# Kernel optimization log

Measured on AMD Instinct MI355X. Metric: run time of the kernel, lower is better.

## Reference

```python
import jax, jax.numpy as jnp
import numpy as np

B, D_IN, D_HID, D_OUT, E, TOP_K = 4096, 1024, 4096, 1024, 8, 2


def setup_inputs() -> dict:
    key = jax.random.key(0)
    ks = jax.random.split(key, 7)
    s_in = 1.0 / np.sqrt(D_IN)
    s_hid = 1.0 / np.sqrt(D_HID)
    return {
        "x": jax.random.normal(ks[0], (B, D_IN), jnp.float32),
        "Wg": jax.random.uniform(ks[1], (D_IN, E), jnp.float32, -s_in, s_in),
        "bg": jax.random.uniform(ks[2], (E,), jnp.float32, -s_in, s_in),
        "W1": jax.random.uniform(ks[3], (E, D_IN, D_HID), jnp.float32, -s_in, s_in),
        "b1": jax.random.uniform(ks[4], (E, D_HID), jnp.float32, -s_in, s_in),
        "W2": jax.random.uniform(ks[5], (E, D_HID, D_OUT), jnp.float32, -s_hid, s_hid),
        "b2": jax.random.uniform(ks[6], (E, D_OUT), jnp.float32, -s_hid, s_hid),
    }


def reference(x, Wg, bg, W1, b1, W2, b2):
    # Gating: [B, E]
    gate_logits = x @ Wg + bg
    # Top-k routing (values sorted descending, same as torch.topk)
    topk_logits, topk_idx = jax.lax.top_k(gate_logits, TOP_K)  # [B, K]
    topk_w = jax.nn.softmax(topk_logits, axis=-1)  # [B, K]

    # Dense per-expert FFN for all tokens (reference form of grouped GEMM)
    h = jax.nn.relu(jnp.einsum("bi,eih->beh", x, W1) + b1[None])  # [B, E, H]
    y = jnp.einsum("beh,eho->beo", h, W2) + b2[None]              # [B, E, O]

    # Gather selected experts' outputs and combine with routing weights
    y_sel = jnp.take_along_axis(y, topk_idx[:, :, None], axis=1)  # [B, K, O]
    output = jnp.sum(topk_w[:, :, None] * y_sel, axis=1)          # [B, O]

    # Load-balance auxiliary loss
    gates = jax.nn.softmax(gate_logits, axis=-1)
    expert_usage = gates.mean(axis=0)
    load_balance_loss = E * jnp.sum(expert_usage ** 2)
    return output, load_balance_loss
```

## Files before the change

kernel.cpp:

```cpp
#include <hip/hip_runtime.h>
#include <hip/hip_fp16.h>

#define BTOK  4096
#define D_IN  1024
#define D_HID 4096
#define D_OUT 1024
#define NE    8
#define PT_MAX 72
#define P_MAX  9216
#define KT1   32
#define NT1M  32
#define KT2M  128
#define NT2   8
#define GB    256

typedef _Float16 half8 __attribute__((ext_vector_type(8)));
typedef _Float16 half4v __attribute__((ext_vector_type(4)));
typedef float    floatx4 __attribute__((ext_vector_type(4)));


__device__ __forceinline__ void g2l16(const void* g, void* s) {
    __builtin_amdgcn_global_load_lds((const __attribute__((address_space(1))) void*)g,
                                     (__attribute__((address_space(3))) void*)s, 16, 0, 0);
}

__global__ __launch_bounds__(256)
void gating_kernel(const float* __restrict__ x, const float* __restrict__ Wg,
                   const float* __restrict__ bg,
                   int* __restrict__ t2i, float* __restrict__ t2w,
                   int* __restrict__ pcnt, float* __restrict__ pusage) {
    __shared__ float wgT[NE * 1024];
    __shared__ float susage[NE];
    __shared__ int   scnt[NE];
    int tid = threadIdx.x;
    if (tid < NE) { susage[tid] = 0.f; scnt[tid] = 0; }
    #pragma unroll
    for (int k = 0; k < 8192; k += 256) {
        int idx = k + tid;
        wgT[(idx & 7) * 1024 + (idx >> 3)] = Wg[idx];
    }
    __syncthreads();
    int wv = tid >> 6, lane = tid & 63;
    for (int tt = 0; tt < 4; ++tt) {
        int t = blockIdx.x * 16 + wv * 4 + tt;
        double part[NE];
        #pragma unroll
        for (int e = 0; e < NE; ++e) part[e] = 0.0;
        #pragma unroll
        for (int j = 0; j < 16; ++j) {
            int i = j * 64 + lane;
            double xv = (double)x[(size_t)t * D_IN + i];
            #pragma unroll
            for (int e = 0; e < NE; ++e) part[e] += xv * (double)wgT[e * 1024 + i];
        }
        #pragma unroll
        for (int e = 0; e < NE; ++e) {
            #pragma unroll
            for (int s = 32; s > 0; s >>= 1) part[e] += __shfl_xor(part[e], s, 64);
        }
        if (lane == 0) {
            float l[NE];
            #pragma unroll
            for (int e = 0; e < NE; ++e) l[e] = (float)part[e] + bg[e];
            float M = l[0];
            #pragma unroll
            for (int e = 1; e < NE; ++e) M = fmaxf(M, l[e]);
            float s = 0.f, g[NE];
            #pragma unroll
            for (int e = 0; e < NE; ++e) { g[e] = __expf(l[e] - M); s += g[e]; }
            float inv = 1.f / s;
            #pragma unroll
            for (int e = 0; e < NE; ++e) atomicAdd(&susage[e], g[e] * inv);
            int i0 = 0; float b0 = l[0];
            #pragma unroll
            for (int e = 1; e < NE; ++e) if (l[e] > b0) { b0 = l[e]; i0 = e; }
            int i1 = -1; float b1v = -1e30f;
            #pragma unroll
            for (int e = 0; e < NE; ++e) if (e != i0 && l[e] > b1v) { b1v = l[e]; i1 = e; }
            float w0 = 1.f / (1.f + expf(b1v - b0));
            t2i[2 * t] = i0; t2i[2 * t + 1] = i1;
            t2w[2 * t] = w0; t2w[2 * t + 1] = 1.f - w0;
            atomicAdd(&scnt[i0], 1);
            atomicAdd(&scnt[i1], 1);
        }
    }
    __syncthreads();
    if (tid < NE) {
        pcnt[blockIdx.x * NE + tid] = scnt[tid];
        pusage[blockIdx.x * NE + tid] = susage[tid];
    }
}

__global__ void scan_kernel(const int* __restrict__ pcnt, const float* __restrict__ pusage,
                            int* __restrict__ meta, float* __restrict__ out_loss) {
    int lane = threadIdx.x;
    int e = lane & 7, b0 = lane >> 3;
    int c = 0; float u = 0.f;
    for (int b = b0; b < GB; b += 8) { c += pcnt[b * 8 + e]; u += pusage[b * 8 + e]; }
    #pragma unroll
    for (int s = 8; s < 64; s <<= 1) { c += __shfl_xor(c, s, 64); u += __shfl_xor(u, s, 64); }
    int cAll[NE]; float uAll[NE];
    #pragma unroll
    for (int q = 0; q < NE; ++q) { cAll[q] = __shfl(c, q, 64); uAll[q] = __shfl(u, q, 64); }
    if (lane == 0) {
        int* cnt = meta; int* cursor = meta + 8; int* offs = meta + 16;
        int* tile2e = meta + 24; int* ntiles = meta + 96;
        int run = 0;
        for (int q = 0; q < NE; ++q) {
            cnt[q] = cAll[q];
            offs[q] = run; cursor[q] = run;
            int ntl = (cAll[q] + 127) >> 7;
            int tb = run >> 7;
            for (int i = 0; i < ntl; ++i) tile2e[tb + i] = q;
            run += ntl << 7;
        }
        ntiles[0] = run >> 7;
        float loss = 0.f;
        for (int q = 0; q < NE; ++q) { float uu = uAll[q] / (float)BTOK; loss += uu * uu; }
        out_loss[0] = (float)NE * loss;
    }
}

__global__ void fill_kernel(int* __restrict__ ptok) {
    ptok[blockIdx.x * 256 + threadIdx.x] = 0;
}

__global__ void scatter_kernel(const int* __restrict__ t2i, int* __restrict__ cursor,
                               int* __restrict__ ptok, int* __restrict__ pslot) {
    __shared__ int lcnt[NE], base[NE];
    int tid = threadIdx.x;
    if (tid < NE) lcnt[tid] = 0;
    __syncthreads();
    int t = blockIdx.x * 256 + tid;
    int e0 = t2i[2 * t], e1 = t2i[2 * t + 1];
    int l0 = atomicAdd(&lcnt[e0], 1);
    int l1 = atomicAdd(&lcnt[e1], 1);
    __syncthreads();
    if (tid < NE) base[tid] = atomicAdd(&cursor[tid], lcnt[tid]);
    __syncthreads();
    int s0 = base[e0] + l0, s1 = base[e1] + l1;
    ptok[s0] = t; ptok[s1] = t;
    pslot[2 * t] = s0; pslot[2 * t + 1] = s1;
}

__global__ void gather_x_kernel(const float* __restrict__ x, const int* __restrict__ ptok,
                                _Float16* __restrict__ xt) {
    int k0 = blockIdx.x, ptile = blockIdx.y;
    int t = threadIdx.x;
    int m = t >> 1, kb = (t & 1) * 16;
    int tok = ptok[ptile * 128 + m];
    const float* src = x + (size_t)tok * D_IN + k0 * 32 + kb;
    float4 v0 = *(const float4*)(src);
    float4 v1 = *(const float4*)(src + 4);
    float4 v2 = *(const float4*)(src + 8);
    float4 v3 = *(const float4*)(src + 12);
    half8 o0, o1;
    o0[0]=(_Float16)v0.x; o0[1]=(_Float16)v0.y; o0[2]=(_Float16)v0.z; o0[3]=(_Float16)v0.w;
    o0[4]=(_Float16)v1.x; o0[5]=(_Float16)v1.y; o0[6]=(_Float16)v1.z; o0[7]=(_Float16)v1.w;
    o1[0]=(_Float16)v2.x; o1[1]=(_Float16)v2.y; o1[2]=(_Float16)v2.z; o1[3]=(_Float16)v2.w;
    o1[4]=(_Float16)v3.x; o1[5]=(_Float16)v3.y; o1[6]=(_Float16)v3.z; o1[7]=(_Float16)v3.w;
    _Float16* dst = xt + ((size_t)ptile * KT1 + k0) * 4096 + t * 16;
    *(half8*)dst = o0;
    *(half8*)(dst + 8) = o1;
}

__global__ void wtile_kernel(const float* __restrict__ W, _Float16* __restrict__ Wt,
                             int Ktot, int Ntot, int KT, int NT) {
    int k0 = blockIdx.x, ntb = blockIdx.y, e = blockIdx.z;
    int t = threadIdx.x;
    int nl = t >> 1, kb = (t & 1) * 16;
    const float* src = W + ((size_t)e * Ktot + k0 * 32 + kb) * Ntot + ntb * 128 + nl;
    float v[16];
    #pragma unroll
    for (int j = 0; j < 16; ++j) v[j] = src[(size_t)j * Ntot];
    half8 o0, o1;
    #pragma unroll
    for (int j = 0; j < 8; ++j) { o0[j] = (_Float16)v[j]; o1[j] = (_Float16)v[j + 8]; }
    _Float16* dst = Wt + (((size_t)e * NT + ntb) * KT + k0) * 4096 + t * 16;
    *(half8*)dst = o0;
    *(half8*)(dst + 8) = o1;
}

__global__ __launch_bounds__(256, 3)
void gemm1_kernel(const _Float16* __restrict__ xt, const _Float16* __restrict__ W1t,
                  const float* __restrict__ b1, _Float16* __restrict__ ht,
                  const int* __restrict__ meta) {
    int ptile = blockIdx.x;
    if (ptile >= meta[96]) return;
    int nt = blockIdx.y;
    int e = meta[24 + ptile];

    __shared__ __align__(16) _Float16 Asm[2][128 * 32];
    __shared__ __align__(16) _Float16 Bsm[2][128 * 32];

    int tid = threadIdx.x;
    int wave = tid >> 6, lane = tid & 63;
    const _Float16* Abase = xt + (size_t)ptile * KT1 * 4096;
    const _Float16* Bbase = W1t + ((size_t)(e * NT1M + nt) * KT1) * 4096;
    int stg = wave * 512 + lane * 8;

    floatx4 acc[4][4] = {};
    int lr = lane & 15, lq = lane >> 4;
    int wm = (wave & 1) * 64, wn = (wave >> 1) * 64;

    g2l16(Abase + stg,        &Asm[0][wave * 512]);
    g2l16(Abase + stg + 2048, &Asm[0][wave * 512 + 2048]);
    g2l16(Bbase + stg,        &Bsm[0][wave * 512]);
    g2l16(Bbase + stg + 2048, &Bsm[0][wave * 512 + 2048]);
    __syncthreads();

    int ct = 0;
    for (int k0 = 0; k0 < KT1; ++k0) {
        if (k0 + 1 < KT1) {
            const _Float16* aG = Abase + (size_t)(k0 + 1) * 4096 + stg;
            const _Float16* bG = Bbase + (size_t)(k0 + 1) * 4096 + stg;
            int nb = ct ^ 1;
            g2l16(aG,        &Asm[nb][wave * 512]);
            g2l16(aG + 2048, &Asm[nb][wave * 512 + 2048]);
            g2l16(bG,        &Bsm[nb][wave * 512]);
            g2l16(bG + 2048, &Bsm[nb][wave * 512 + 2048]);
        }
        const _Float16* As = Asm[ct];
        const _Float16* Bs = Bsm[ct];
        half8 af[4], bf[4];
        #pragma unroll
        for (int f = 0; f < 4; ++f) {
            af[f] = *(const half8*)&As[(wm + f * 16 + lr) * 32 + lq * 8];
            bf[f] = *(const half8*)&Bs[(wn + f * 16 + lr) * 32 + lq * 8];
        }
        #pragma unroll
        for (int mf = 0; mf < 4; ++mf)
            #pragma unroll
            for (int nf = 0; nf < 4; ++nf)
                acc[mf][nf] = __builtin_amdgcn_mfma_f32_16x16x32_f16(af[mf], bf[nf], acc[mf][nf], 0, 0, 0);
        __syncthreads();
        ct ^= 1;
    }

    const float* b1e = b1 + (size_t)e * D_HID;
    #pragma unroll
    for (int mf = 0; mf < 4; ++mf) {
        #pragma unroll
        for (int v = 0; v < 4; ++v) {
            int m = wm + mf * 16 + lq * 4 + v;
            #pragma unroll
            for (int nf = 0; nf < 4; ++nf) {
                int hl = nt * 128 + wn + nf * 16 + lr;
                float val = acc[mf][nf][v] + b1e[hl];
                ht[((size_t)ptile * KT2M + (hl >> 5)) * 4096 + m * 32 + (hl & 31)]
                    = (_Float16)fmaxf(val, 0.f);
            }
        }
    }
}

__global__ __launch_bounds__(256, 3)
void gemm2_kernel(const _Float16* __restrict__ ht, const _Float16* __restrict__ W2t,
                  _Float16* __restrict__ y, const int* __restrict__ meta) {
    int ptile = blockIdx.x;
    if (ptile >= meta[96]) return;
    int nt = blockIdx.y;
    int e = meta[24 + ptile];

    __shared__ __align__(16) _Float16 Asm[2][128 * 32];
    __shared__ __align__(16) _Float16 Bsm[2][128 * 32];

    int tid = threadIdx.x;
    int wave = tid >> 6, lane = tid & 63;
    const _Float16* Abase = ht + (size_t)ptile * KT2M * 4096;
    const _Float16* Bbase = W2t + ((size_t)(e * NT2 + nt) * KT2M) * 4096;
    int stg = wave * 512 + lane * 8;

    floatx4 acc[4][4] = {};
    int lr = lane & 15, lq = lane >> 4;
    int wm = (wave & 1) * 64, wn = (wave >> 1) * 64;

    g2l16(Abase + stg,        &Asm[0][wave * 512]);
    g2l16(Abase + stg + 2048, &Asm[0][wave * 512 + 2048]);
    g2l16(Bbase + stg,        &Bsm[0][wave * 512]);
    g2l16(Bbase + stg + 2048, &Bsm[0][wave * 512 + 2048]);
    __syncthreads();

    int ct = 0;
    for (int k0 = 0; k0 < KT2M; ++k0) {
        if (k0 + 1 < KT2M) {
            const _Float16* aG = Abase + (size_t)(k0 + 1) * 4096 + stg;
            const _Float16* bG = Bbase + (size_t)(k0 + 1) * 4096 + stg;
            int nb = ct ^ 1;
            g2l16(aG,        &Asm[nb][wave * 512]);
            g2l16(aG + 2048, &Asm[nb][wave * 512 + 2048]);
            g2l16(bG,        &Bsm[nb][wave * 512]);
            g2l16(bG + 2048, &Bsm[nb][wave * 512 + 2048]);
        }
        const _Float16* As = Asm[ct];
        const _Float16* Bs = Bsm[ct];
        half8 af[4], bf[4];
        #pragma unroll
        for (int f = 0; f < 4; ++f) {
            af[f] = *(const half8*)&As[(wm + f * 16 + lr) * 32 + lq * 8];
            bf[f] = *(const half8*)&Bs[(wn + f * 16 + lr) * 32 + lq * 8];
        }
        #pragma unroll
        for (int mf = 0; mf < 4; ++mf)
            #pragma unroll
            for (int nf = 0; nf < 4; ++nf)
                acc[mf][nf] = __builtin_amdgcn_mfma_f32_16x16x32_f16(af[mf], bf[nf], acc[mf][nf], 0, 0, 0);
        __syncthreads();
        ct ^= 1;
    }

    #pragma unroll
    for (int mf = 0; mf < 4; ++mf) {
        #pragma unroll
        for (int v = 0; v < 4; ++v) {
            int m = wm + mf * 16 + lq * 4 + v;
            #pragma unroll
            for (int nf = 0; nf < 4; ++nf) {
                int c = nt * 128 + wn + nf * 16 + lr;
                y[(size_t)(ptile * 128 + m) * D_OUT + c] = (_Float16)acc[mf][nf][v];
            }
        }
    }
}

__global__ void combine_kernel(const _Float16* __restrict__ y, const float* __restrict__ b2,
                               const int* __restrict__ t2i, const float* __restrict__ t2w,
                               const int* __restrict__ pslot, float* __restrict__ out) {
    int t = blockIdx.x;
    int c = threadIdx.x * 4;
    int e0 = t2i[2 * t], e1 = t2i[2 * t + 1];
    float w0 = t2w[2 * t], w1 = t2w[2 * t + 1];
    size_t s0 = (size_t)pslot[2 * t] * D_OUT + c;
    size_t s1 = (size_t)pslot[2 * t + 1] * D_OUT + c;
    half4v a0 = *(const half4v*)(y + s0);
    half4v a1 = *(const half4v*)(y + s1);
    float4 bias0 = *(const float4*)(b2 + (size_t)e0 * D_OUT + c);
    float4 bias1 = *(const float4*)(b2 + (size_t)e1 * D_OUT + c);
    float4 o;
    o.x = w0 * ((float)a0[0] + bias0.x) + w1 * ((float)a1[0] + bias1.x);
    o.y = w0 * ((float)a0[1] + bias0.y) + w1 * ((float)a1[1] + bias1.y);
    o.z = w0 * ((float)a0[2] + bias0.z) + w1 * ((float)a1[2] + bias1.z);
    o.w = w0 * ((float)a0[3] + bias0.w) + w1 * ((float)a1[3] + bias1.w);
    *(float4*)(out + (size_t)t * D_OUT + c) = o;
}

extern "C" void kernel_launch(void* const* d_in, const int* in_sizes, int n_in,
                              void* d_out, int out_size, void* d_ws, size_t ws_size,
                              hipStream_t stream) {
    const float* x  = (const float*)d_in[0];
    const float* Wg = (const float*)d_in[1];
    const float* bg = (const float*)d_in[2];
    const float* W1 = (const float*)d_in[3];
    const float* b1 = (const float*)d_in[4];
    const float* W2 = (const float*)d_in[5];
    const float* b2 = (const float*)d_in[6];
    float* out = (float*)d_out;

    char* ws = (char*)d_ws;
    _Float16* xt     = (_Float16*)(ws);
    _Float16* W1t    = (_Float16*)(ws + 18874368ull);
    _Float16* W2t    = (_Float16*)(ws + 85983232ull);
    _Float16* ht     = (_Float16*)(ws + 153092096ull);
    _Float16* y      = (_Float16*)(ws + 228589568ull);
    int*      t2i    = (int*)(ws + 247463936ull);
    float*    t2w    = (float*)(ws + 247496704ull);
    int*      ptok   = (int*)(ws + 247529472ull);
    int*      pslot  = (int*)(ws + 247566336ull);
    int*      meta   = (int*)(ws + 247599104ull);
    int*      pcnt   = (int*)(ws + 247599616ull);
    float*    pusage = (float*)(ws + 247607808ull);
    int* cursor = meta + 8;

    hipMemsetAsync(meta, 0, 512, stream);

    gating_kernel<<<GB, 256, 0, stream>>>(x, Wg, bg, t2i, t2w, pcnt, pusage);
    scan_kernel<<<1, 64, 0, stream>>>(pcnt, pusage, meta, out + (size_t)BTOK * D_OUT);
    fill_kernel<<<36, 256, 0, stream>>>(ptok);
    scatter_kernel<<<16, 256, 0, stream>>>(t2i, cursor, ptok, pslot);
    gather_x_kernel<<<dim3(KT1, PT_MAX), 256, 0, stream>>>(x, ptok, xt);

    wtile_kernel<<<dim3(KT1, NT1M, 8), 256, 0, stream>>>(W1, W1t, D_IN, D_HID, KT1, NT1M);
    wtile_kernel<<<dim3(KT2M, NT2, 8), 256, 0, stream>>>(W2, W2t, D_HID, D_OUT, KT2M, NT2);

    gemm1_kernel<<<dim3(PT_MAX, NT1M), 256, 0, stream>>>(xt, W1t, b1, ht, meta);
    gemm2_kernel<<<dim3(PT_MAX, NT2), 256, 0, stream>>>(ht, W2t, y, meta);

    combine_kernel<<<BTOK, 256, 0, stream>>>(y, b2, t2i, t2w, pslot, out);
}
```

Measured before the change: 602.6 us.

## Enlarge grouped GEMM tiles to 256x256 with 8 waves and deeper pipelining

Both expert GEMMs move from 128x128 tiles with 4 waves to 256x256 tiles with 8 waves per block. Each k-step now stages 64 K-columns in two halves and prefetches two stages ahead, using explicit waitcnt/barrier control, register double-buffering of fragments and s_setprio around the MFMA bursts. Expert segments are padded to multiples of 256 rows so every macro tile belongs to one expert, and the workspace layout grows to match. The aim is more data reuse per global and LDS load and better overlap of loads with MFMAs, at the cost of more padding work, fewer blocks in the grid and higher register pressure.

Result: slower. 633.1 us (+5.1%).

```diff
diff --git a/kernel.cpp b/kernel.cpp
--- a/kernel.cpp
+++ b/kernel.cpp
@@ -6,11 +6,12 @@
 #define D_HID 4096
 #define D_OUT 1024
 #define NE    8
-#define PT_MAX 72
-#define P_MAX  9216
+#define PT_MAX 80
+#define PT2_MAX 40
+#define P_MAX  10240
 #define KT1   32
 #define NT1M  32
-#define KT2M  128
+#define KT2C  128
 #define NT2   8
 #define GB    256
 
@@ -104,12 +105,12 @@
     for (int q = 0; q < NE; ++q) { cAll[q] = __shfl(c, q, 64); uAll[q] = __shfl(u, q, 64); }
     if (lane == 0) {
         int* cnt = meta; int* cursor = meta + 8; int* offs = meta + 16;
-        int* tile2e = meta + 24; int* ntiles = meta + 96;
+        int* tile2e = meta + 24; int* ntiles = meta + 104;
         int run = 0;
         for (int q = 0; q < NE; ++q) {
             cnt[q] = cAll[q];
             offs[q] = run; cursor[q] = run;
-            int ntl = (cAll[q] + 127) >> 7;
+            int ntl = ((cAll[q] + 255) >> 8) << 1;
             int tb = run >> 7;
             for (int i = 0; i < ntl; ++i) tile2e[tb + i] = q;
             run += ntl << 7;
@@ -181,143 +182,172 @@
     *(half8*)(dst + 8) = o1;
 }
 
-__global__ __launch_bounds__(256, 3)
+template<int NKT>
+__device__ __forceinline__ void gemm_core(
+    const _Float16* __restrict__ Ab, const _Float16* __restrict__ Bb, size_t aS,
+    _Float16 (&LA)[2][2][2 * 4096], _Float16 (&LB)[2][2][2 * 4096],
+    int wave, int lane, floatx4 (&acc)[8][4])
+{
+    int wr = wave >> 2, wc = wave & 3;
+    int lr = lane & 15, lq = lane >> 4;
+    int go  = wave * 512 + lane * 8;
+    int aro = wr * 4096;
+    int bro = (wc >> 1) * 4096 + (wc & 1) * 2048;
+    int fo  = lr * 32 + lq * 8;
+
+#define STG(kt, s, h) do { \
+    const _Float16* ga_ = Ab + (size_t)((kt) * 2 + (h)) * 4096 + go; \
+    const _Float16* gb_ = Bb + (size_t)((kt) * 2 + (h)) * 4096 + go; \
+    g2l16(ga_,      &LA[s][h][wave * 512]); \
+    g2l16(ga_ + aS, &LA[s][h][4096 + wave * 512]); \
+    g2l16(gb_,      &LB[s][h][wave * 512]); \
+    g2l16(gb_ + aS, &LB[s][h][4096 + wave * 512]); \
+} while (0)
+
+    half8 af[8], bf[4];
+
+    STG(0, 0, 0); STG(0, 0, 1); STG(1, 1, 0); STG(1, 1, 1);
+    asm volatile("s_waitcnt vmcnt(8)" ::: "memory");
+    __builtin_amdgcn_s_barrier();
+    {
+        const _Float16* Ar = &LA[0][0][aro];
+        const _Float16* Br = &LB[0][0][bro];
+        #pragma unroll
+        for (int mf = 0; mf < 8; ++mf) af[mf] = *(const half8*)(Ar + mf * 512 + fo);
+        #pragma unroll
+        for (int nf = 0; nf < 4; ++nf) bf[nf] = *(const half8*)(Br + nf * 512 + fo);
+    }
+    asm volatile("s_waitcnt lgkmcnt(0)" ::: "memory");
+    __builtin_amdgcn_s_barrier();
+
+    for (int kt = 0; kt < NKT; ++kt) {
+        int s = kt & 1;
+        bool st = (kt + 2 < NKT);
+
+        if (st) STG(kt + 2, s, 0);
+        {
+            const _Float16* Ar = &LA[s][1][aro];
+            const _Float16* Br = &LB[s][1][bro];
+            __builtin_amdgcn_s_setprio(1);
+            #pragma unroll
+            for (int mf = 0; mf < 8; ++mf) {
+                #pragma unroll
+                for (int nf = 0; nf < 4; ++nf)
+                    acc[mf][nf] = __builtin_amdgcn_mfma_f32_16x16x32_f16(af[mf], bf[nf], acc[mf][nf], 0, 0, 0);
+                if (mf == 7) {
+                    #pragma unroll
+                    for (int nf = 0; nf < 4; ++nf) bf[nf] = *(const half8*)(Br + nf * 512 + fo);
+                }
+                af[mf] = *(const half8*)(Ar + mf * 512 + fo);
+            }
+            __builtin_amdgcn_s_setprio(0);
+        }
+        asm volatile("s_waitcnt lgkmcnt(0)" ::: "memory");
+        __builtin_amdgcn_s_barrier();
+
+        if (st) STG(kt + 2, s, 1);
+        bool nx = (kt + 1 < NKT);
+        if (nx) {
+            if (st) { asm volatile("s_waitcnt vmcnt(8)" ::: "memory"); }
+            else    { asm volatile("s_waitcnt vmcnt(0)" ::: "memory"); }
+        }
+        {
+            const _Float16* Ar = &LA[s ^ 1][0][aro];
+            const _Float16* Br = &LB[s ^ 1][0][bro];
+            __builtin_amdgcn_s_setprio(1);
+            #pragma unroll
+            for (int mf = 0; mf < 8; ++mf) {
+                #pragma unroll
+                for (int nf = 0; nf < 4; ++nf)
+                    acc[mf][nf] = __builtin_amdgcn_mfma_f32_16x16x32_f16(af[mf], bf[nf], acc[mf][nf], 0, 0, 0);
+                if (mf == 7 && nx) {
+                    #pragma unroll
+                    for (int nf2 = 0; nf2 < 4; ++nf2) bf[nf2] = *(const half8*)(Br + nf2 * 512 + fo);
+                }
+                if (nx) af[mf] = *(const half8*)(Ar + mf * 512 + fo);
+            }
+            __builtin_amdgcn_s_setprio(0);
+        }
+        asm volatile("s_waitcnt lgkmcnt(0)" ::: "memory");
+        __builtin_amdgcn_s_barrier();
+    }
+#undef STG
+}
+
+__global__ __launch_bounds__(512, 2)
 void gemm1_kernel(const _Float16* __restrict__ xt, const _Float16* __restrict__ W1t,
                   const float* __restrict__ b1, _Float16* __restrict__ ht,
                   const int* __restrict__ meta) {
-    int ptile = blockIdx.x;
-    if (ptile >= meta[96]) return;
-    int nt = blockIdx.y;
-    int e = meta[24 + ptile];
-
-    __shared__ __align__(16) _Float16 Asm[2][128 * 32];
-    __shared__ __align__(16) _Float16 Bsm[2][128 * 32];
-
-    int tid = threadIdx.x;
-    int wave = tid >> 6, lane = tid & 63;
-    const _Float16* Abase = xt + (size_t)ptile * KT1 * 4096;
-    const _Float16* Bbase = W1t + ((size_t)(e * NT1M + nt) * KT1) * 4096;
-    int stg = wave * 512 + lane * 8;
-
-    floatx4 acc[4][4] = {};
+    int mc = blockIdx.x;
+    if (mc * 2 >= meta[104]) return;
+    int nc = blockIdx.y;
+    int e = meta[24 + mc * 2];
+
+    __shared__ __align__(16) _Float16 LA[2][2][2 * 4096];
+    __shared__ __align__(16) _Float16 LB[2][2][2 * 4096];
+
+    int tid = threadIdx.x, wave = tid >> 6, lane = tid & 63;
+    int wr = wave >> 2, wc = wave & 3;
     int lr = lane & 15, lq = lane >> 4;
-    int wm = (wave & 1) * 64, wn = (wave >> 1) * 64;
-
-    g2l16(Abase + stg,        &Asm[0][wave * 512]);
-    g2l16(Abase + stg + 2048, &Asm[0][wave * 512 + 2048]);
-    g2l16(Bbase + stg,        &Bsm[0][wave * 512]);
-    g2l16(Bbase + stg + 2048, &Bsm[0][wave * 512 + 2048]);
-    __syncthreads();
-
-    int ct = 0;
-    for (int k0 = 0; k0 < KT1; ++k0) {
-        if (k0 + 1 < KT1) {
-            const _Float16* aG = Abase + (size_t)(k0 + 1) * 4096 + stg;
-            const _Float16* bG = Bbase + (size_t)(k0 + 1) * 4096 + stg;
-            int nb = ct ^ 1;
-            g2l16(aG,        &Asm[nb][wave * 512]);
-            g2l16(aG + 2048, &Asm[nb][wave * 512 + 2048]);
-            g2l16(bG,        &Bsm[nb][wave * 512]);
-            g2l16(bG + 2048, &Bsm[nb][wave * 512 + 2048]);
-        }
-        const _Float16* As = Asm[ct];
-        const _Float16* Bs = Bsm[ct];
-        half8 af[4], bf[4];
-        #pragma unroll
-        for (int f = 0; f < 4; ++f) {
-            af[f] = *(const half8*)&As[(wm + f * 16 + lr) * 32 + lq * 8];
-            bf[f] = *(const half8*)&Bs[(wn + f * 16 + lr) * 32 + lq * 8];
-        }
-        #pragma unroll
-        for (int mf = 0; mf < 4; ++mf)
-            #pragma unroll
-            for (int nf = 0; nf < 4; ++nf)
-                acc[mf][nf] = __builtin_amdgcn_mfma_f32_16x16x32_f16(af[mf], bf[nf], acc[mf][nf], 0, 0, 0);
-        __syncthreads();
-        ct ^= 1;
-    }
-
-    const float* b1e = b1 + (size_t)e * D_HID;
-    #pragma unroll
-    for (int mf = 0; mf < 4; ++mf) {
+
+    const _Float16* Ab = xt + (size_t)(mc * 2) * (KT1 * 4096);
+    const _Float16* Bb = W1t + (size_t)(e * NT1M + nc * 2) * (KT1 * 4096);
+    size_t aS = (size_t)KT1 * 4096;
+
+    floatx4 acc[8][4] = {};
+    gemm_core<16>(Ab, Bb, aS, LA, LB, wave, lane, acc);
+
+    const float* b1e = b1 + (size_t)e * D_HID + nc * 256 + wc * 64;
+    #pragma unroll
+    for (int mf = 0; mf < 8; ++mf) {
         #pragma unroll
         for (int v = 0; v < 4; ++v) {
-            int m = wm + mf * 16 + lq * 4 + v;
+            int mm = wr * 128 + mf * 16 + lq * 4 + v;
+            int ptile = mc * 2 + (mm >> 7);
+            int ml = mm & 127;
             #pragma unroll
             for (int nf = 0; nf < 4; ++nf) {
-                int hl = nt * 128 + wn + nf * 16 + lr;
-                float val = acc[mf][nf][v] + b1e[hl];
-                ht[((size_t)ptile * KT2M + (hl >> 5)) * 4096 + m * 32 + (hl & 31)]
+                int hl = nc * 256 + wc * 64 + nf * 16 + lr;
+                float val = acc[mf][nf][v] + b1e[nf * 16 + lr];
+                ht[((size_t)ptile * KT2C + (hl >> 5)) * 4096 + ml * 32 + (hl & 31)]
                     = (_Float16)fmaxf(val, 0.f);
             }
         }
     }
 }
 
-__global__ __launch_bounds__(256, 3)
+__global__ __launch_bounds__(512, 2)
 void gemm2_kernel(const _Float16* __restrict__ ht, const _Float16* __restrict__ W2t,
                   _Float16* __restrict__ y, const int* __restrict__ meta) {
-    int ptile = blockIdx.x;
-    if (ptile >= meta[96]) return;
-    int nt = blockIdx.y;
-    int e = meta[24 + ptile];
-
-    __shared__ __align__(16) _Float16 Asm[2][128 * 32];
-    __shared__ __align__(16) _Float16 Bsm[2][128 * 32];
-
-    int tid = threadIdx.x;
-    int wave = tid >> 6, lane = tid & 63;
-    const _Float16* Abase = ht + (size_t)ptile * KT2M * 4096;
-    const _Float16* Bbase = W2t + ((size_t)(e * NT2 + nt) * KT2M) * 4096;
-    int stg = wave * 512 + lane * 8;
-
-    floatx4 acc[4][4] = {};
+    int mc = blockIdx.x;
+    if (mc * 2 >= meta[104]) return;
+    int nc = blockIdx.y;
+    int e = meta[24 + mc * 2];
+
+    __shared__ __align__(16) _Float16 LA[2][2][2 * 4096];
+    __shared__ __align__(16) _Float16 LB[2][2][2 * 4096];
+
+    int tid = threadIdx.x, wave = tid >> 6, lane = tid & 63;
+    int wr = wave >> 2, wc = wave & 3;
     int lr = lane & 15, lq = lane >> 4;
-    int wm = (wave & 1) * 64, wn = (wave >> 1) * 64;
-
-    g2l16(Abase + stg,        &Asm[0][wave * 512]);
-    g2l16(Abase + stg + 2048, &Asm[0][wave * 512 + 2048]);
-    g2l16(Bbase + stg,        &Bsm[0][wave * 512]);
-    g2l16(Bbase + stg + 2048, &Bsm[0][wave * 512 + 2048]);
-    __syncthreads();
-
-    int ct = 0;
-    for (int k0 = 0; k0 < KT2M; ++k0) {
-        if (k0 + 1 < KT2M) {
-            const _Float16* aG = Abase + (size_t)(k0 + 1) * 4096 + stg;
-            const _Float16* bG = Bbase + (size_t)(k0 + 1) * 4096 + stg;
-            int nb = ct ^ 1;
-            g2l16(aG,        &Asm[nb][wave * 512]);
-            g2l16(aG + 2048, &Asm[nb][wave * 512 + 2048]);
-            g2l16(bG,        &Bsm[nb][wave * 512]);
-            g2l16(bG + 2048, &Bsm[nb][wave * 512 + 2048]);
-        }
-        const _Float16* As = Asm[ct];
-        const _Float16* Bs = Bsm[ct];
-        half8 af[4], bf[4];
-        #pragma unroll
-        for (int f = 0; f < 4; ++f) {
-            af[f] = *(const half8*)&As[(wm + f * 16 + lr) * 32 + lq * 8];
-            bf[f] = *(const half8*)&Bs[(wn + f * 16 + lr) * 32 + lq * 8];
-        }
-        #pragma unroll
-        for (int mf = 0; mf < 4; ++mf)
-            #pragma unroll
-            for (int nf = 0; nf < 4; ++nf)
-                acc[mf][nf] = __builtin_amdgcn_mfma_f32_16x16x32_f16(af[mf], bf[nf], acc[mf][nf], 0, 0, 0);
-        __syncthreads();
-        ct ^= 1;
-    }
-
-    #pragma unroll
-    for (int mf = 0; mf < 4; ++mf) {
+
+    const _Float16* Ab = ht + (size_t)(mc * 2) * (KT2C * 4096);
+    const _Float16* Bb = W2t + (size_t)(e * NT2 + nc * 2) * (KT2C * 4096);
+    size_t aS = (size_t)KT2C * 4096;
+
+    floatx4 acc[8][4] = {};
+    gemm_core<64>(Ab, Bb, aS, LA, LB, wave, lane, acc);
+
+    #pragma unroll
+    for (int mf = 0; mf < 8; ++mf) {
         #pragma unroll
         for (int v = 0; v < 4; ++v) {
-            int m = wm + mf * 16 + lq * 4 + v;
+            int mm = wr * 128 + mf * 16 + lq * 4 + v;
+            int row = mc * 256 + mm;
             #pragma unroll
             for (int nf = 0; nf < 4; ++nf) {
-                int c = nt * 128 + wn + nf * 16 + lr;
-                y[(size_t)(ptile * 128 + m) * D_OUT + c] = (_Float16)acc[mf][nf][v];
+                int col = nc * 256 + wc * 64 + nf * 16 + lr;
+                y[(size_t)row * D_OUT + col] = (_Float16)acc[mf][nf][v];
             }
         }
     }
@@ -358,32 +388,32 @@
 
     char* ws = (char*)d_ws;
     _Float16* xt     = (_Float16*)(ws);
-    _Float16* W1t    = (_Float16*)(ws + 18874368ull);
-    _Float16* W2t    = (_Float16*)(ws + 85983232ull);
-    _Float16* ht     = (_Float16*)(ws + 153092096ull);
-    _Float16* y      = (_Float16*)(ws + 228589568ull);
-    int*      t2i    = (int*)(ws + 247463936ull);
-    float*    t2w    = (float*)(ws + 247496704ull);
-    int*      ptok   = (int*)(ws + 247529472ull);
-    int*      pslot  = (int*)(ws + 247566336ull);
-    int*      meta   = (int*)(ws + 247599104ull);
-    int*      pcnt   = (int*)(ws + 247599616ull);
-    float*    pusage = (float*)(ws + 247607808ull);
+    _Float16* W1t    = (_Float16*)(ws + 20971520ull);
+    _Float16* W2t    = (_Float16*)(ws + 88080384ull);
+    _Float16* ht     = (_Float16*)(ws + 155189248ull);
+    _Float16* y      = (_Float16*)(ws + 239075328ull);
+    int*      t2i    = (int*)(ws + 260046848ull);
+    float*    t2w    = (float*)(ws + 260079616ull);
+    int*      ptok   = (int*)(ws + 260112384ull);
+    int*      pslot  = (int*)(ws + 260153344ull);
+    int*      meta   = (int*)(ws + 260186112ull);
+    int*      pcnt   = (int*)(ws + 260186624ull);
+    float*    pusage = (float*)(ws + 260194816ull);
     int* cursor = meta + 8;
 
     hipMemsetAsync(meta, 0, 512, stream);
 
     gating_kernel<<<GB, 256, 0, stream>>>(x, Wg, bg, t2i, t2w, pcnt, pusage);
     scan_kernel<<<1, 64, 0, stream>>>(pcnt, pusage, meta, out + (size_t)BTOK * D_OUT);
-    fill_kernel<<<36, 256, 0, stream>>>(ptok);
+    fill_kernel<<<PT2_MAX, 256, 0, stream>>>(ptok);
     scatter_kernel<<<16, 256, 0, stream>>>(t2i, cursor, ptok, pslot);
     gather_x_kernel<<<dim3(KT1, PT_MAX), 256, 0, stream>>>(x, ptok, xt);
 
     wtile_kernel<<<dim3(KT1, NT1M, 8), 256, 0, stream>>>(W1, W1t, D_IN, D_HID, KT1, NT1M);
-    wtile_kernel<<<dim3(KT2M, NT2, 8), 256, 0, stream>>>(W2, W2t, D_HID, D_OUT, KT2M, NT2);
-
-    gemm1_kernel<<<dim3(PT_MAX, NT1M), 256, 0, stream>>>(xt, W1t, b1, ht, meta);
-    gemm2_kernel<<<dim3(PT_MAX, NT2), 256, 0, stream>>>(ht, W2t, y, meta);
+    wtile_kernel<<<dim3(KT2C, NT2, 8), 256, 0, stream>>>(W2, W2t, D_HID, D_OUT, KT2C, NT2);
+
+    gemm1_kernel<<<dim3(PT2_MAX, 16), 512, 0, stream>>>(xt, W1t, b1, ht, meta);
+    gemm2_kernel<<<dim3(PT2_MAX, 4), 512, 0, stream>>>(ht, W2t, y, meta);
 
     combine_kernel<<<BTOK, 256, 0, stream>>>(y, b2, t2i, t2w, pslot, out);
 }
```
